# Kernel optimization log

Measured on AMD Instinct MI355X. Metric: run time of the kernel, lower is better.

## Reference

```python
import jax, jax.numpy as jnp
import numpy as np
import math

B, T, C = 4, 2048, 1024
H = 16
HD = C // H


def setup_inputs() -> dict:
    key = jax.random.key(0)
    k1, k2, k3 = jax.random.split(key, 3)
    sc = 0.02
    return {
        "x": jax.random.normal(k1, (B, T, C), dtype=jnp.float32),
        "w_qkv": jax.random.normal(k2, (3 * C, C), dtype=jnp.float32) * sc,
        "b_qkv": jnp.zeros((3 * C,), dtype=jnp.float32),
        "w_proj": jax.random.normal(k3, (C, C), dtype=jnp.float32) * sc,
        "b_proj": jnp.zeros((C,), dtype=jnp.float32),
    }


def reference(x, w_qkv, b_qkv, w_proj, b_proj):
    b, t, c = x.shape
    qkv = x @ w_qkv.T + b_qkv            # [B,T,3C]
    q, k, v = jnp.split(qkv, 3, axis=2)
    # [B,T,C] -> [B,H,T,HD]
    def heads(z):
        return z.reshape(b, t, H, HD).transpose(0, 2, 1, 3)
    q, k, v = heads(q), heads(k), heads(v)
    att = jnp.einsum('bhqd,bhkd->bhqk', q, k) / math.sqrt(HD)
    causal = jnp.tril(jnp.ones((t, t), dtype=bool))
    att = jnp.where(causal[None, None], att, -jnp.inf)
    att = jax.nn.softmax(att, axis=-1)   # dropout p=0 (eval)
    y = jnp.einsum('bhqk,bhkd->bhqd', att, v)
    y = y.transpose(0, 2, 1, 3).reshape(b, t, c)
    return y @ w_proj.T + b_proj
```

## Files before the change

### kernel.cpp

```cpp
#include <hip/hip_runtime.h>
#include <hip/hip_bf16.h>

#define B_ 4
#define T_ 2048
#define C_ 1024
#define H_ 16
#define HD_ 64
#define M_ (B_*T_)

typedef __attribute__((ext_vector_type(8))) short short8;
typedef __attribute__((ext_vector_type(4))) float f32x4;
typedef __attribute__((ext_vector_type(16))) float f32x16;
typedef __attribute__((ext_vector_type(4))) unsigned int u32x4;
typedef unsigned short u16;
typedef unsigned int u32;

__device__ __forceinline__ u16 f2bf(float f){
  unsigned int x = __builtin_bit_cast(unsigned int, f);
  x += 0x7fffu + ((x >> 16) & 1u);
  return (u16)(x >> 16);
}

__device__ __forceinline__ u32 cvtpk(float lo, float hi){
  u32 r;
  asm("v_cvt_pk_bf16_f32 %0, %1, %2" : "=v"(r) : "v"(lo), "v"(hi));
  return r;
}

#define GLOAD_LDS(gsrc, ldst) \
  __builtin_amdgcn_global_load_lds((const __attribute__((address_space(1))) u32*)(gsrc), \
                                   (__attribute__((address_space(3))) u32*)(ldst), 16, 0, 0)

__global__ __launch_bounds__(256) void cvt_kernel(const float* __restrict__ in,
                                                  u16* __restrict__ out, int n4){
  int i = blockIdx.x * 256 + threadIdx.x;
  if (i >= n4) return;
  float4 f = reinterpret_cast<const float4*>(in)[i];
  ushort4 u;
  u.x = f2bf(f.x); u.y = f2bf(f.y); u.z = f2bf(f.z); u.w = f2bf(f.w);
  reinterpret_cast<ushort4*>(out)[i] = u;
}

template<int MODE>
__global__ __launch_bounds__(256)
void gemm_bt(const u16* __restrict__ A, const u16* __restrict__ Bt,
             const float* __restrict__ bias, float* __restrict__ Cf,
             u16* __restrict__ Qo, u16* __restrict__ Ko, u16* __restrict__ Vo,
             int N, int K)
{
  __shared__ u16 As[128 * 64];
  __shared__ u16 Bs[128 * 64];
  const int tid = threadIdx.x;
  const int wave = tid >> 6, lane = tid & 63;
  const int lo = lane & 15, hi = lane >> 4;
  const int wm = (wave >> 1) * 64, wn = (wave & 1) * 64;
  const long bm = (long)blockIdx.y * 128, bn = (long)blockIdx.x * 128;

  f32x4 acc[4][4];
  #pragma unroll
  for (int i = 0; i < 4; i++)
    #pragma unroll
    for (int j = 0; j < 4; j++)
      acc[i][j] = (f32x4){0.f, 0.f, 0.f, 0.f};

  for (int k0 = 0; k0 < K; k0 += 64){
    if (k0) __syncthreads();
    #pragma unroll
    for (int j = 0; j < 4; j++){
      int chunk = j * 256 + tid;
      int row = chunk >> 3, cc = (chunk & 7) * 8;
      GLOAD_LDS(&A [(bm + row) * K + k0 + cc], &As[chunk * 8]);
      GLOAD_LDS(&Bt[(bn + row) * K + k0 + cc], &Bs[chunk * 8]);
    }
    __syncthreads();
    #pragma unroll
    for (int kk = 0; kk < 64; kk += 32){
      short8 af[4], bf[4];
      #pragma unroll
      for (int mi = 0; mi < 4; mi++)
        af[mi] = *reinterpret_cast<const short8*>(&As[(wm + mi*16 + lo) * 64 + kk + hi*8]);
      #pragma unroll
      for (int ni = 0; ni < 4; ni++)
        bf[ni] = *reinterpret_cast<const short8*>(&Bs[(wn + ni*16 + lo) * 64 + kk + hi*8]);
      #pragma unroll
      for (int mi = 0; mi < 4; mi++)
        #pragma unroll
        for (int ni = 0; ni < 4; ni++)
          acc[mi][ni] = __builtin_amdgcn_mfma_f32_16x16x32_bf16(af[mi], bf[ni], acc[mi][ni], 0, 0, 0);
    }
  }

  #pragma unroll
  for (int mi = 0; mi < 4; mi++){
    #pragma unroll
    for (int ni = 0; ni < 4; ni++){
      #pragma unroll
      for (int rg = 0; rg < 4; rg++){
        long rowg = bm + wm + mi*16 + hi*4 + rg;
        long colg = bn + wn + ni*16 + lo;
        float v = acc[mi][ni][rg] + bias[colg];
        if (MODE == 0){
          int part = (int)(colg >> 10), cc = (int)(colg & 1023);
          int h = cc >> 6, d = cc & 63;
          long b = rowg >> 11, t = rowg & 2047;
          if (part == 0) v *= 0.18033688f;
          u16* dst = (part == 0) ? Qo : ((part == 1) ? Ko : Vo);
          dst[(((b << 4) + h) * 2048 + t) * 64 + d] = f2bf(v);
        } else {
          Cf[rowg * (long)N + colg] = v;
        }
      }
    }
  }
}

__global__ __launch_bounds__(256)
void vtrans_kernel(const u16* __restrict__ V, u16* __restrict__ Vt){
  __shared__ u16 Ls[64][72];
  const int bh = blockIdx.y;
  const int t0 = blockIdx.x * 64;
  const u16* Vb = V + ((size_t)bh * 2048 + t0) * 64;
  u16* Ob = Vt + (size_t)bh * 64 * 2048 + t0;
  const int r = threadIdx.x >> 3;
  const int c = (threadIdx.x & 7) * 8;
  #pragma unroll
  for (int rr = 0; rr < 64; rr += 32){
    int row = r + rr;
    *reinterpret_cast<short8*>(&Ls[row][c ^ (((row >> 4) & 3) << 4)]) =
      *reinterpret_cast<const short8*>(&Vb[(size_t)row * 64 + c]);
  }
  __syncthreads();
  const int d  = threadIdx.x >> 2;
  const int tc = (threadIdx.x & 3) * 16;
  const int v  = ((tc >> 4) & 3) << 4;
  short8 o0, o1;
  #pragma unroll
  for (int j = 0; j < 8; j++) o0[j] = (short)Ls[tc + j][d ^ v];
  #pragma unroll
  for (int j = 0; j < 8; j++) o1[j] = (short)Ls[tc + 8 + j][d ^ v];
  *reinterpret_cast<short8*>(&Ob[(size_t)d * 2048 + tc]) = o0;
  *reinterpret_cast<short8*>(&Ob[(size_t)d * 2048 + tc + 8]) = o1;
}

__global__ __launch_bounds__(256, 2)
void attn_kernel(const u16* __restrict__ Q, const u16* __restrict__ K,
                 const u16* __restrict__ Vt, u16* __restrict__ Y)
{
  const int blk = blockIdx.x;
  const int bh = (blk & 7) * 8 + ((blk >> 3) & 7);
  const int qg = 15 - (blk >> 6);
  const int tid = threadIdx.x, wave = tid >> 6, lane = tid & 63;
  const int l31 = lane & 31, h5 = lane >> 5;
  const int qc = qg * 4 + wave;
  const int q0w = qc * 32;
  const int qrow = q0w + l31;
  const u16* Qb = Q  + (size_t)bh * 2048 * 64;
  const u16* Kb = K  + (size_t)bh * 2048 * 64;
  const u16* Vb = Vt + (size_t)bh * 64 * 2048;

  short8 qf[4];
  #pragma unroll
  for (int ks = 0; ks < 4; ks++)
    qf[ks] = *reinterpret_cast<const short8*>(&Qb[(size_t)qrow * 64 + ks * 16 + h5 * 8]);

  f32x16 o0, o1;
  #pragma unroll
  for (int i = 0; i < 16; i++){ o0[i] = 0.f; o1[i] = 0.f; }
  float m = -1e30f, l = 0.f;

  const int F = qc >> 1;

  for (int jt = 0; jt <= F; jt++){
    const int k0 = jt << 6;

    short8 kf0[4], kf1[4];
    #pragma unroll
    for (int ks = 0; ks < 4; ks++){
      kf0[ks] = *reinterpret_cast<const short8*>(&Kb[(size_t)(k0 + l31) * 64 + ks * 16 + h5 * 8]);
      kf1[ks] = *reinterpret_cast<const short8*>(&Kb[(size_t)(k0 + 32 + l31) * 64 + ks * 16 + h5 * 8]);
    }
    f32x16 st0, st1;
    #pragma unroll
    for (int i = 0; i < 16; i++){ st0[i] = 0.f; st1[i] = 0.f; }
    __builtin_amdgcn_s_setprio(1);
    #pragma unroll
    for (int ks = 0; ks < 4; ks++)
      st0 = __builtin_amdgcn_mfma_f32_32x32x16_bf16(kf0[ks], qf[ks], st0, 0, 0, 0);
    #pragma unroll
    for (int ks = 0; ks < 4; ks++)
      st1 = __builtin_amdgcn_mfma_f32_32x32x16_bf16(kf1[ks], qf[ks], st1, 0, 0, 0);
    __builtin_amdgcn_s_setprio(0);

    short8 vf0[4], vf1[4];
    #pragma unroll
    for (int ks = 0; ks < 4; ks++){
      vf0[ks] = *reinterpret_cast<const short8*>(&Vb[(size_t)l31 * 2048 + k0 + ks * 16 + h5 * 8]);
      vf1[ks] = *reinterpret_cast<const short8*>(&Vb[(size_t)(32 + l31) * 2048 + k0 + ks * 16 + h5 * 8]);
    }

    if (jt == F){
      #pragma unroll
      for (int r = 0; r < 16; r++){
        int kvr = k0 + (r & 3) + 8 * (r >> 2) + 4 * h5;
        if (kvr > qrow)      st0[r] = -1e30f;
        if (kvr + 32 > qrow) st1[r] = -1e30f;
      }
    }

    float t[16];
    #pragma unroll
    for (int r = 0; r < 16; r++) t[r] = fmaxf(st0[r], st1[r]);
    #pragma unroll
    for (int s = 8; s > 0; s >>= 1)
      #pragma unroll
      for (int r = 0; r < 8; r++) if (r < s) t[r] = fmaxf(t[r], t[r + s]);
    float rm = fmaxf(t[0], __shfl_xor(t[0], 32));
    float mn = fmaxf(m, rm);
    float alpha = __builtin_amdgcn_exp2f(m - mn);
    m = mn;
    float rs = 0.f;
    #pragma unroll
    for (int r = 0; r < 16; r++){
      st0[r] = __builtin_amdgcn_exp2f(st0[r] - mn);
      st1[r] = __builtin_amdgcn_exp2f(st1[r] - mn);
      rs += st0[r] + st1[r];
    }
    rs += __shfl_xor(rs, 32);
    l = l * alpha + rs;
    #pragma unroll
    for (int i = 0; i < 16; i++){ o0[i] *= alpha; o1[i] *= alpha; }

    short8 pa[4];
    #pragma unroll
    for (int ks2 = 0; ks2 < 4; ks2++){
      const f32x16& sv = (ks2 < 2) ? st0 : st1;
      const int gg = 8 * (ks2 & 1);
      u32 w0 = cvtpk(sv[gg + 0], sv[gg + 1]);
      u32 w1 = cvtpk(sv[gg + 2], sv[gg + 3]);
      u32 w2 = cvtpk(sv[gg + 4], sv[gg + 5]);
      u32 w3 = cvtpk(sv[gg + 6], sv[gg + 7]);
      u32 sa = h5 ? w0 : w2;
      u32 sb = h5 ? w1 : w3;
      u32 ra = (u32)__shfl_xor((int)sa, 32);
      u32 rb = (u32)__shfl_xor((int)sb, 32);
      u32x4 pw;
      pw.x = h5 ? ra : w0;
      pw.y = h5 ? rb : w1;
      pw.z = h5 ? w2 : ra;
      pw.w = h5 ? w3 : rb;
      pa[ks2] = __builtin_bit_cast(short8, pw);
    }

    __builtin_amdgcn_s_setprio(1);
    #pragma unroll
    for (int ks = 0; ks < 4; ks++)
      o0 = __builtin_amdgcn_mfma_f32_32x32x16_bf16(vf0[ks], pa[ks], o0, 0, 0, 0);
    #pragma unroll
    for (int ks = 0; ks < 4; ks++)
      o1 = __builtin_amdgcn_mfma_f32_32x32x16_bf16(vf1[ks], pa[ks], o1, 0, 0, 0);
    __builtin_amdgcn_s_setprio(0);
  }

  const int b = bh >> 4, h = bh & 15;
  const float inv = 1.f / l;
  u16* Yr = Y + ((size_t)(b * 2048 + qrow)) * 1024 + h * 64;
  #pragma unroll
  for (int rq = 0; rq < 4; rq++){
    ushort4 ua, ub;
    #pragma unroll
    for (int e = 0; e < 4; e++){
      ((u16*)&ua)[e] = f2bf(o0[rq * 4 + e] * inv);
      ((u16*)&ub)[e] = f2bf(o1[rq * 4 + e] * inv);
    }
    *reinterpret_cast<ushort4*>(&Yr[rq * 8 + h5 * 4])      = ua;
    *reinterpret_cast<ushort4*>(&Yr[32 + rq * 8 + h5 * 4]) = ub;
  }
}

extern "C" void kernel_launch(void* const* d_in, const int* in_sizes, int n_in,
                              void* d_out, int out_size, void* d_ws, size_t ws_size,
                              hipStream_t stream)
{
  const float* x      = (const float*)d_in[0];
  const float* w_qkv  = (const float*)d_in[1];
  const float* b_qkv  = (const float*)d_in[2];
  const float* w_proj = (const float*)d_in[3];
  const float* b_proj = (const float*)d_in[4];
  float* out = (float*)d_out;

  char* ws = (char*)d_ws;
  u16* xb     = (u16*)(ws);
  u16* wqkvb  = (u16*)(ws + (16u << 20));
  u16* wprojb = (u16*)(ws + (22u << 20));
  u16* qb     = (u16*)(ws + (24u << 20));
  u16* kb     = (u16*)(ws + (40u << 20));
  u16* vb     = (u16*)(ws + (56u << 20));
  u16* yb     = (u16*)(ws + (72u << 20));
  u16* vtb    = xb;

  int nx  = B_ * T_ * C_ / 4;
  int nw1 = 3 * C_ * C_ / 4;
  int nw2 = C_ * C_ / 4;
  cvt_kernel<<<(nx  + 255) / 256, 256, 0, stream>>>(x,      xb,     nx);
  cvt_kernel<<<(nw1 + 255) / 256, 256, 0, stream>>>(w_qkv,  wqkvb,  nw1);
  cvt_kernel<<<(nw2 + 255) / 256, 256, 0, stream>>>(w_proj, wprojb, nw2);

  dim3 g1(3072 / 128, M_ / 128);
  gemm_bt<0><<<g1, 256, 0, stream>>>(xb, wqkvb, b_qkv, nullptr, qb, kb, vb, 3072, C_);

  dim3 gt(T_ / 64, B_ * H_);
  vtrans_kernel<<<gt, 256, 0, stream>>>(vb, vtb);

  attn_kernel<<<1024, 256, 0, stream>>>(qb, kb, vtb, yb);

  dim3 g2(1024 / 128, M_ / 128);
  gemm_bt<1><<<g2, 256, 0, stream>>>(yb, wprojb, b_proj, out, nullptr, nullptr, nullptr, C_, C_);
}
```

Before: 260.4 us.

## Split long causal attention rows across two waves with partial-softmax combine kernel

The attention kernel moves from 256-thread blocks covering 4 query chunks to 128-thread blocks. For the 32 longest query chunks, the KV range is split between two waves, each writing an unnormalized bf16 partial output plus running max and sum. The remaining chunks are processed whole, two per block. A new combine kernel merges the split partials with rescaling, which balances causal workload across blocks. The cost is an extra launch, extra global traffic for partials stored in reused workspace, and bf16 rounding of the unnormalized partials.

```diff
diff --git a/kernel.cpp b/kernel.cpp
--- a/kernel.cpp
+++ b/kernel.cpp
@@ -19,6 +19,11 @@
   unsigned int x = __builtin_bit_cast(unsigned int, f);
   x += 0x7fffu + ((x >> 16) & 1u);
   return (u16)(x >> 16);
+}
+
+__device__ __forceinline__ float b2f(u16 u){
+  u32 x = ((u32)u) << 16;
+  return __builtin_bit_cast(float, x);
 }
 
 __device__ __forceinline__ u32 cvtpk(float lo, float hi){
@@ -142,16 +147,36 @@
   *reinterpret_cast<short8*>(&Ob[(size_t)d * 2048 + tc + 8]) = o1;
 }
 
-__global__ __launch_bounds__(256, 2)
+__global__ __launch_bounds__(128, 4)
 void attn_kernel(const u16* __restrict__ Q, const u16* __restrict__ K,
-                 const u16* __restrict__ Vt, u16* __restrict__ Y)
+                 const u16* __restrict__ Vt, u16* __restrict__ Y,
+                 u16* __restrict__ Opart, float* __restrict__ Ml)
 {
   const int blk = blockIdx.x;
   const int bh = (blk & 7) * 8 + ((blk >> 3) & 7);
-  const int qg = 15 - (blk >> 6);
+  const int u = blk >> 6;
   const int tid = threadIdx.x, wave = tid >> 6, lane = tid & 63;
   const int l31 = lane & 31, h5 = lane >> 5;
-  const int qc = qg * 4 + wave;
+
+  int qc, jt0, jt1, half;
+  bool split;
+  if (u < 32){
+    split = true;
+    qc = 63 - u;
+    half = wave;
+    int nt = (qc >> 1) + 1;
+    int h0 = (nt + 1) >> 1;
+    jt0 = half ? h0 : 0;
+    jt1 = half ? nt : h0;
+  } else {
+    split = false;
+    int v = 47 - u;
+    qc = 2 * v + wave;
+    half = 0;
+    jt0 = 0;
+    jt1 = (qc >> 1) + 1;
+  }
+  const int F = qc >> 1;
   const int q0w = qc * 32;
   const int qrow = q0w + l31;
   const u16* Qb = Q  + (size_t)bh * 2048 * 64;
@@ -168,9 +193,7 @@
   for (int i = 0; i < 16; i++){ o0[i] = 0.f; o1[i] = 0.f; }
   float m = -1e30f, l = 0.f;
 
-  const int F = qc >> 1;
-
-  for (int jt = 0; jt <= F; jt++){
+  for (int jt = jt0; jt < jt1; jt++){
     const int k0 = jt << 6;
 
     short8 kf0[4], kf1[4];
@@ -261,20 +284,73 @@
     __builtin_amdgcn_s_setprio(0);
   }
 
+  if (!split){
+    const int b = bh >> 4, h = bh & 15;
+    const float inv = 1.f / l;
+    u16* Yr = Y + ((size_t)(b * 2048 + qrow)) * 1024 + h * 64;
+    #pragma unroll
+    for (int rq = 0; rq < 4; rq++){
+      ushort4 ua, ub;
+      #pragma unroll
+      for (int e = 0; e < 4; e++){
+        ((u16*)&ua)[e] = f2bf(o0[rq * 4 + e] * inv);
+        ((u16*)&ub)[e] = f2bf(o1[rq * 4 + e] * inv);
+      }
+      *reinterpret_cast<ushort4*>(&Yr[rq * 8 + h5 * 4])      = ua;
+      *reinterpret_cast<ushort4*>(&Yr[32 + rq * 8 + h5 * 4]) = ub;
+    }
+  } else {
+    const int unit = (bh * 32 + (qc - 32)) * 2 + half;
+    u16* Or = Opart + (size_t)unit * 2048 + l31 * 64;
+    #pragma unroll
+    for (int rq = 0; rq < 4; rq++){
+      ushort4 ua, ub;
+      #pragma unroll
+      for (int e = 0; e < 4; e++){
+        ((u16*)&ua)[e] = f2bf(o0[rq * 4 + e]);
+        ((u16*)&ub)[e] = f2bf(o1[rq * 4 + e]);
+      }
+      *reinterpret_cast<ushort4*>(&Or[rq * 8 + h5 * 4])      = ua;
+      *reinterpret_cast<ushort4*>(&Or[32 + rq * 8 + h5 * 4]) = ub;
+    }
+    if (h5 == 0){
+      Ml[(size_t)unit * 64 + l31 * 2 + 0] = m;
+      Ml[(size_t)unit * 64 + l31 * 2 + 1] = l;
+    }
+  }
+}
+
+__global__ __launch_bounds__(256)
+void combine_kernel(const u16* __restrict__ Opart, const float* __restrict__ Ml,
+                    u16* __restrict__ Y)
+{
+  const int cb = blockIdx.x;
+  const int bh = cb >> 5, qcrel = cb & 31;
+  const int t = threadIdx.x;
+  const int r = t >> 3, d8 = (t & 7) * 8;
+  const int u0 = (bh * 32 + qcrel) * 2, u1 = u0 + 1;
+
+  float m0 = Ml[(size_t)u0 * 64 + r * 2], l0 = Ml[(size_t)u0 * 64 + r * 2 + 1];
+  float m1 = Ml[(size_t)u1 * 64 + r * 2], l1 = Ml[(size_t)u1 * 64 + r * 2 + 1];
+  float mS = fmaxf(m0, m1);
+  float a0 = __builtin_amdgcn_exp2f(m0 - mS);
+  float a1 = __builtin_amdgcn_exp2f(m1 - mS);
+  float inv = 1.f / (l0 * a0 + l1 * a1);
+
+  short8 O0 = *reinterpret_cast<const short8*>(&Opart[(size_t)u0 * 2048 + r * 64 + d8]);
+  short8 O1 = *reinterpret_cast<const short8*>(&Opart[(size_t)u1 * 2048 + r * 64 + d8]);
+  ushort4 oa, ob;
+  #pragma unroll
+  for (int j = 0; j < 8; j++){
+    float y = (b2f((u16)O0[j]) * a0 + b2f((u16)O1[j]) * a1) * inv;
+    ((u16*)(j < 4 ? &oa : &ob))[j & 3] = f2bf(y);
+  }
+  const int qc = 32 + qcrel;
+  const int qrow = qc * 32 + r;
   const int b = bh >> 4, h = bh & 15;
-  const float inv = 1.f / l;
-  u16* Yr = Y + ((size_t)(b * 2048 + qrow)) * 1024 + h * 64;
-  #pragma unroll
-  for (int rq = 0; rq < 4; rq++){
-    ushort4 ua, ub;
-    #pragma unroll
-    for (int e = 0; e < 4; e++){
-      ((u16*)&ua)[e] = f2bf(o0[rq * 4 + e] * inv);
-      ((u16*)&ub)[e] = f2bf(o1[rq * 4 + e] * inv);
-    }
-    *reinterpret_cast<ushort4*>(&Yr[rq * 8 + h5 * 4])      = ua;
-    *reinterpret_cast<ushort4*>(&Yr[32 + rq * 8 + h5 * 4]) = ub;
-  }
+  u16* Yr = Y + ((size_t)(b * 2048 + qrow)) * 1024 + h * 64 + d8;
+  *reinterpret_cast<ushort4*>(Yr)     = oa;
+  *reinterpret_cast<ushort4*>(Yr + 4) = ob;
 }
 
 extern "C" void kernel_launch(void* const* d_in, const int* in_sizes, int n_in,
@@ -297,6 +373,8 @@
   u16* vb     = (u16*)(ws + (56u << 20));
   u16* yb     = (u16*)(ws + (72u << 20));
   u16* vtb    = xb;
+  u16* opart  = vb;
+  float* ml   = (float*)wqkvb;
 
   int nx  = B_ * T_ * C_ / 4;
   int nw1 = 3 * C_ * C_ / 4;
@@ -311,7 +389,8 @@
   dim3 gt(T_ / 64, B_ * H_);
   vtrans_kernel<<<gt, 256, 0, stream>>>(vb, vtb);
 
-  attn_kernel<<<1024, 256, 0, stream>>>(qb, kb, vtb, yb);
+  attn_kernel<<<3072, 128, 0, stream>>>(qb, kb, vtb, yb, opart, ml);
+  combine_kernel<<<2048, 256, 0, stream>>>(opart, ml, yb);
 
   dim3 g2(1024 / 128, M_ / 128);
   gemm_bt<1><<<g2, 256, 0, stream>>>(yb, wprojb, b_proj, out, nullptr, nullptr, nullptr, C_, C_);
```

Measured after the change: 312.4 us. +20.0%, slower.
